# Kernel optimization log

Measured on AMD Instinct MI355X. Metric: run time of the kernel, lower is better.

## Reference

```python
import jax, jax.numpy as jnp
import numpy as np

HID = 4096; NH = 32; NKV = 8; HD = 128; EPS = 1e-6; BASE = 10000.0

def _rmsnorm(x, w):
    # RMSNorm over last (head_dim) axis
    return x * jax.lax.rsqrt(jnp.mean(x * x, axis=-1, keepdims=True) + EPS) * w

def _rope(x, positions):
    # neox-style rotary on (b, s, h, HD): rotate halves
    half = HD // 2
    inv_freq = 1.0 / (BASE ** (jnp.arange(0, HD, 2, dtype=jnp.float32) / HD))  # (half,)
    ang = positions.astype(jnp.float32)[:, None] * inv_freq                    # (s, half)
    cos = jnp.cos(ang)[None, :, None, :]
    sin = jnp.sin(ang)[None, :, None, :]
    x1, x2 = x[..., :half], x[..., half:]
    return jnp.concatenate([x1 * cos - x2 * sin, x2 * cos + x1 * sin], axis=-1)

def setup_inputs() -> dict:
    key = jax.random.key(0)
    k0, k1, k2 = jax.random.split(key, 3)
    b, s = 4, 1024
    return {
        "h_shard": jax.random.normal(k0, (b, s, HID), jnp.float32),
        "positions": jnp.arange(s, dtype=jnp.int32),
        "w_qkv": jax.random.normal(k1, (NH * HD + 2 * NKV * HD, HID), jnp.float32) * 0.02,
        "w_o": jax.random.normal(k2, (HID, NH * HD), jnp.float32) * 0.02,
        "q_norm_w": jnp.ones((HD,), jnp.float32),
        "k_norm_w": jnp.ones((HD,), jnp.float32),
    }

def reference(h_shard, positions, w_qkv, w_o, q_norm_w, k_norm_w):
    b, s, _ = h_shard.shape
    q_sz, kv_sz = NH * HD, NKV * HD
    # fused QKV projection (world_size=1 -> ag_mm is a plain matmul x @ W.T)
    qkv = h_shard @ w_qkv.T                                   # (b, s, q_sz + 2*kv_sz)
    q = qkv[..., :q_sz].reshape(b, s, NH, HD)
    k = qkv[..., q_sz:q_sz + kv_sz].reshape(b, s, NKV, HD)
    v = qkv[..., q_sz + kv_sz:].reshape(b, s, NKV, HD)
    # per-head RMSNorm then RoPE on q/k (Qwen3 ordering)
    q = _rope(_rmsnorm(q, q_norm_w), positions)
    k = _rope(_rmsnorm(k, k_norm_w), positions)
    # GQA SDPA without materializing repeated KV: group query heads per kv head
    g = NH // NKV
    qg = q.reshape(b, s, NKV, g, HD)
    scores = jnp.einsum('bskgd,btkd->bkgst', qg, k) / jnp.sqrt(jnp.float32(HD))
    causal = jnp.tril(jnp.ones((s, s), dtype=bool))
    scores = jnp.where(causal, scores, -jnp.inf)
    probs = jax.nn.softmax(scores, axis=-1)
    attn = jnp.einsum('bkgst,btkd->bskgd', probs, v).reshape(b, s, q_sz)
    # output projection (mm_rs -> plain matmul for world_size=1)
    return attn @ w_o.T
```

## Files before the change

### kernel.cpp

```cpp
#include <hip/hip_runtime.h>

typedef __bf16 bf16;
typedef __bf16 bf16x4 __attribute__((ext_vector_type(4)));
typedef __bf16 bf16x8 __attribute__((ext_vector_type(8)));
typedef float f32x4 __attribute__((ext_vector_type(4)));

#define HID 4096
#define QKV_N 6144
#define NTOK 4096

__device__ __forceinline__ void gload_lds16(const bf16* g, bf16* l) {
  __builtin_amdgcn_global_load_lds(
      (__attribute__((address_space(1))) void*)(g),
      (__attribute__((address_space(3))) void*)(l), 16, 0, 0);
}

__global__ void cvt_kernel(const float4* __restrict__ s, bf16x4* __restrict__ d) {
  int i = blockIdx.x * blockDim.x + threadIdx.x;
  float4 v = s[i];
  bf16x4 o;
  o[0] = (bf16)v.x; o[1] = (bf16)v.y; o[2] = (bf16)v.z; o[3] = (bf16)v.w;
  d[i] = o;
}

template <typename OutT>
__global__ __launch_bounds__(256) void gemm_bt(
    const bf16* __restrict__ A, const bf16* __restrict__ Bm,
    OutT* __restrict__ C, int M, int N, int K)
{
  __shared__ bf16 As[128 * 64];
  __shared__ bf16 Bs[128 * 64];
  const int tid = threadIdx.x;
  const int w = tid >> 6, l = tid & 63;
  const int quad = l >> 4, lane16 = l & 15;
  const int row0 = blockIdx.y * 128, col0 = blockIdx.x * 128;
  const int wm = (w & 1) * 64, wn = (w >> 1) * 64;
  const int lrow = l >> 3;
  const int lkswz = ((l & 7) ^ lrow) * 8;
  const int sw = lane16 & 7;

  f32x4 acc[4][4];
#pragma unroll
  for (int a = 0; a < 4; ++a)
#pragma unroll
    for (int b = 0; b < 4; ++b) acc[a][b] = (f32x4){0.f, 0.f, 0.f, 0.f};

  for (int k0 = 0; k0 < K; k0 += 64) {
#pragma unroll
    for (int r = 0; r < 4; ++r) {
      int i = r * 4 + w;
      gload_lds16(A + (size_t)(row0 + i * 8 + lrow) * K + k0 + lkswz, &As[i * 512 + l * 8]);
      gload_lds16(Bm + (size_t)(col0 + i * 8 + lrow) * K + k0 + lkswz, &Bs[i * 512 + l * 8]);
    }
    __syncthreads();
#pragma unroll
    for (int kk = 0; kk < 2; ++kk) {
      bf16x8 af[4], bfr[4];
#pragma unroll
      for (int im = 0; im < 4; ++im)
        af[im] = *(const bf16x8*)&As[(wm + im * 16 + lane16) * 64 + (((kk * 4 + quad) ^ sw) * 8)];
#pragma unroll
      for (int in_ = 0; in_ < 4; ++in_)
        bfr[in_] = *(const bf16x8*)&Bs[(wn + in_ * 16 + lane16) * 64 + (((kk * 4 + quad) ^ sw) * 8)];
#pragma unroll
      for (int im = 0; im < 4; ++im)
#pragma unroll
        for (int in_ = 0; in_ < 4; ++in_)
          acc[im][in_] = __builtin_amdgcn_mfma_f32_16x16x32_bf16(af[im], bfr[in_], acc[im][in_], 0, 0, 0);
    }
    __syncthreads();
  }
#pragma unroll
  for (int im = 0; im < 4; ++im) {
#pragma unroll
    for (int r = 0; r < 4; ++r) {
      int row = row0 + wm + im * 16 + quad * 4 + r;
      OutT* cp = C + (size_t)row * N + col0 + wn;
#pragma unroll
      for (int in_ = 0; in_ < 4; ++in_)
        cp[in_ * 16 + lane16] = (OutT)acc[im][in_][r];
    }
  }
}

__global__ __launch_bounds__(256) void norm_rope_kernel(
    bf16* __restrict__ qkv, const int* __restrict__ pos,
    const float* __restrict__ qw, const float* __restrict__ kw)
{
  int g = blockIdx.x * 4 + (threadIdx.x >> 6);
  int tok = g / 40;
  int slot = g % 40;
  int d = threadIdx.x & 63;
  bf16* base;
  const float* w;
  if (slot < 32) { base = qkv + (size_t)tok * QKV_N + slot * 128; w = qw; }
  else           { base = qkv + (size_t)tok * QKV_N + HID + (slot - 32) * 128; w = kw; }
  float x1 = (float)base[d], x2 = (float)base[d + 64];
  float ss = x1 * x1 + x2 * x2;
#pragma unroll
  for (int m = 1; m < 64; m <<= 1) ss += __shfl_xor(ss, m, 64);
  float rn = rsqrtf(ss * (1.0f / 128.0f) + 1e-6f);
  x1 = x1 * rn * w[d];
  x2 = x2 * rn * w[d + 64];
  int p = pos[tok & 1023];
  float invf = exp2f(-0.20762050593045952f * (float)d);
  float ang = (float)p * invf;
  float sn, c;
  sincosf(ang, &sn, &c);
  base[d]      = (bf16)(x1 * c - x2 * sn);
  base[d + 64] = (bf16)(x2 * c + x1 * sn);
}

__global__ __launch_bounds__(256) void flash_kernel(
    const bf16* __restrict__ qkv, bf16* __restrict__ attn)
{
  __shared__ bf16 Qs[64 * 128];
  __shared__ bf16 Ks[64 * 128];
  __shared__ bf16 Vt[128 * 72];
  __shared__ bf16 Ps[4][16 * 72];

  const int qt = blockIdx.x;
  const int bh = blockIdx.y;
  const int batch = bh >> 5;
  const int qh = bh & 31;
  const int kvh = qh >> 2;
  const int tid = threadIdx.x;
  const int w = tid >> 6, l = tid & 63;
  const int quad = l >> 4, lane16 = l & 15;
  const int sw = lane16 & 7;
  const size_t tok0 = (size_t)batch * 1024;
  const int q0 = qt * 64;

#pragma unroll
  for (int r = 0; r < 4; ++r) {
    int i = r * 4 + w;
    int rloc = i * 4 + (l >> 4);
    int o = (l & 15) ^ (rloc & 7);
    const bf16* g = qkv + (tok0 + q0 + rloc) * QKV_N + qh * 128 + o * 8;
    gload_lds16(g, &Qs[i * 512 + l * 8]);
  }

  f32x4 O[8];
#pragma unroll
  for (int id = 0; id < 8; ++id) O[id] = (f32x4){0.f, 0.f, 0.f, 0.f};
  float m_run[4], l_run[4];
#pragma unroll
  for (int r = 0; r < 4; ++r) { m_run[r] = -1e30f; l_run[r] = 0.f; }

  const float scale = 0.08838834764831845f;

  for (int j = 0; j <= qt; ++j) {
#pragma unroll
    for (int r = 0; r < 4; ++r) {
      int i = r * 4 + w;
      int rloc = i * 4 + (l >> 4);
      int o = (l & 15) ^ (rloc & 7);
      const bf16* g = qkv + (tok0 + j * 64 + rloc) * QKV_N + HID + kvh * 128 + o * 8;
      gload_lds16(g, &Ks[i * 512 + l * 8]);
    }
#pragma unroll
    for (int c = 0; c < 4; ++c) {
      int dg = c * 4 + w;
      int d0 = dg * 8;
      const bf16* g = qkv + (tok0 + j * 64 + l) * QKV_N + HID + 1024 + kvh * 128 + d0;
      bf16x8 v = *(const bf16x8*)g;
#pragma unroll
      for (int e = 0; e < 8; ++e) Vt[(d0 + e) * 72 + l] = v[e];
    }
    __syncthreads();

    f32x4 s[4];
#pragma unroll
    for (int in_ = 0; in_ < 4; ++in_) s[in_] = (f32x4){0.f, 0.f, 0.f, 0.f};
#pragma unroll
    for (int kk = 0; kk < 4; ++kk) {
      bf16x8 a = *(const bf16x8*)&Qs[(w * 16 + lane16) * 128 + (((kk * 4 + quad) ^ sw) * 8)];
#pragma unroll
      for (int in_ = 0; in_ < 4; ++in_) {
        bf16x8 b = *(const bf16x8*)&Ks[(in_ * 16 + lane16) * 128 + (((kk * 4 + quad) ^ sw) * 8)];
        s[in_] = __builtin_amdgcn_mfma_f32_16x16x32_bf16(a, b, s[in_], 0, 0, 0);
      }
    }

#pragma unroll
    for (int r = 0; r < 4; ++r) {
      int q_abs = q0 + w * 16 + quad * 4 + r;
      float rm = -1e30f;
#pragma unroll
      for (int in_ = 0; in_ < 4; ++in_) {
        int t_abs = j * 64 + in_ * 16 + lane16;
        float v = s[in_][r] * scale;
        v = (t_abs <= q_abs) ? v : -1e30f;
        s[in_][r] = v;
        rm = fmaxf(rm, v);
      }
#pragma unroll
      for (int m = 1; m < 16; m <<= 1) rm = fmaxf(rm, __shfl_xor(rm, m, 64));
      float mn = fmaxf(m_run[r], rm);
      float alpha = __expf(m_run[r] - mn);
      m_run[r] = mn;
      float rs = 0.f;
#pragma unroll
      for (int in_ = 0; in_ < 4; ++in_) {
        float pv = __expf(s[in_][r] - mn);
        s[in_][r] = pv;
        rs += pv;
      }
#pragma unroll
      for (int m = 1; m < 16; m <<= 1) rs += __shfl_xor(rs, m, 64);
      l_run[r] = l_run[r] * alpha + rs;
#pragma unroll
      for (int id = 0; id < 8; ++id) O[id][r] *= alpha;
#pragma unroll
      for (int in_ = 0; in_ < 4; ++in_)
        Ps[w][(quad * 4 + r) * 72 + in_ * 16 + lane16] = (bf16)s[in_][r];
    }

#pragma unroll
    for (int kt = 0; kt < 2; ++kt) {
      bf16x8 a = *(const bf16x8*)&Ps[w][lane16 * 72 + kt * 32 + quad * 8];
#pragma unroll
      for (int id = 0; id < 8; ++id) {
        bf16x8 b = *(const bf16x8*)&Vt[(id * 16 + lane16) * 72 + kt * 32 + quad * 8];
        O[id] = __builtin_amdgcn_mfma_f32_16x16x32_bf16(a, b, O[id], 0, 0, 0);
      }
    }
    __syncthreads();
  }

#pragma unroll
  for (int r = 0; r < 4; ++r) {
    float inv = 1.0f / l_run[r];
    int row = q0 + w * 16 + quad * 4 + r;
    bf16* orow = attn + (tok0 + row) * (size_t)HID + qh * 128;
#pragma unroll
    for (int id = 0; id < 8; ++id) orow[id * 16 + lane16] = (bf16)(O[id][r] * inv);
  }
}

extern "C" void kernel_launch(void* const* d_in, const int* in_sizes, int n_in,
                              void* d_out, int out_size, void* d_ws, size_t ws_size,
                              hipStream_t stream) {
  const float* h    = (const float*)d_in[0];
  const int*   pos  = (const int*)d_in[1];
  const float* wqkv = (const float*)d_in[2];
  const float* wo   = (const float*)d_in[3];
  const float* qw   = (const float*)d_in[4];
  const float* kw   = (const float*)d_in[5];
  float* out = (float*)d_out;

  bf16* hb    = (bf16*)d_ws;
  bf16* wqkvb = hb + 16777216;
  bf16* wob   = wqkvb + 25165824;
  bf16* qkvb  = wob + 16777216;
  bf16* attnb = qkvb + 25165824;

  cvt_kernel<<<16384, 256, 0, stream>>>((const float4*)h, (bf16x4*)hb);
  cvt_kernel<<<24576, 256, 0, stream>>>((const float4*)wqkv, (bf16x4*)wqkvb);
  cvt_kernel<<<16384, 256, 0, stream>>>((const float4*)wo, (bf16x4*)wob);

  gemm_bt<bf16><<<dim3(48, 32), 256, 0, stream>>>(hb, wqkvb, qkvb, NTOK, QKV_N, HID);

  norm_rope_kernel<<<NTOK * 40 / 4, 256, 0, stream>>>(qkvb, pos, qw, kw);

  flash_kernel<<<dim3(16, 128), 256, 0, stream>>>(qkvb, attnb);

  gemm_bt<float><<<dim3(32, 32), 256, 0, stream>>>(attnb, wob, out, NTOK, HID, HID);
}
```

Measured before the change: 875.0 us.

## Double-buffer K/V in flash attention and keep Q fragments in registers

The flash attention kernel now double-buffers K and V tiles in LDS, prefetching the next K via async global-to-LDS loads and the next V into registers while the current tile computes. Q fragments are held in registers instead of LDS, V transpose uses an XOR-swizzled layout without padding, causal masking runs only on the diagonal tile, and the q-tile order is reversed for half the heads to balance causal work. This aims to hide global load latency and cut LDS traffic and barriers, at the cost of more LDS and registers, which may lower occupancy.

```diff
diff --git a/kernel.cpp b/kernel.cpp
--- a/kernel.cpp
+++ b/kernel.cpp
@@ -114,13 +114,12 @@
 __global__ __launch_bounds__(256) void flash_kernel(
     const bf16* __restrict__ qkv, bf16* __restrict__ attn)
 {
-  __shared__ bf16 Qs[64 * 128];
-  __shared__ bf16 Ks[64 * 128];
-  __shared__ bf16 Vt[128 * 72];
+  __shared__ bf16 Ks[2][64 * 128];
+  __shared__ bf16 Vt[2][128 * 64];
   __shared__ bf16 Ps[4][16 * 72];
 
-  const int qt = blockIdx.x;
   const int bh = blockIdx.y;
+  const int qt = ((bh >> 4) & 1) ? (15 - blockIdx.x) : blockIdx.x;
   const int batch = bh >> 5;
   const int qh = bh & 31;
   const int kvh = qh >> 2;
@@ -131,13 +130,11 @@
   const size_t tok0 = (size_t)batch * 1024;
   const int q0 = qt * 64;
 
-#pragma unroll
-  for (int r = 0; r < 4; ++r) {
-    int i = r * 4 + w;
-    int rloc = i * 4 + (l >> 4);
-    int o = (l & 15) ^ (rloc & 7);
-    const bf16* g = qkv + (tok0 + q0 + rloc) * QKV_N + qh * 128 + o * 8;
-    gload_lds16(g, &Qs[i * 512 + l * 8]);
+  bf16x8 qf[4];
+  {
+    const bf16* qrow = qkv + (tok0 + q0 + w * 16 + lane16) * QKV_N + qh * 128 + quad * 8;
+#pragma unroll
+    for (int kk = 0; kk < 4; ++kk) qf[kk] = *(const bf16x8*)(qrow + kk * 32);
   }
 
   f32x4 O[8];
@@ -148,49 +145,72 @@
   for (int r = 0; r < 4; ++r) { m_run[r] = -1e30f; l_run[r] = 0.f; }
 
   const float scale = 0.08838834764831845f;
-
-  for (int j = 0; j <= qt; ++j) {
+  bf16x8 vreg[4];
+
+  auto stage_K = [&](int j, int buf) {
 #pragma unroll
     for (int r = 0; r < 4; ++r) {
       int i = r * 4 + w;
       int rloc = i * 4 + (l >> 4);
       int o = (l & 15) ^ (rloc & 7);
       const bf16* g = qkv + (tok0 + j * 64 + rloc) * QKV_N + HID + kvh * 128 + o * 8;
-      gload_lds16(g, &Ks[i * 512 + l * 8]);
-    }
+      gload_lds16(g, &Ks[buf][i * 512 + l * 8]);
+    }
+  };
+  auto load_V = [&](int j) {
 #pragma unroll
     for (int c = 0; c < 4; ++c) {
-      int dg = c * 4 + w;
-      int d0 = dg * 8;
-      const bf16* g = qkv + (tok0 + j * 64 + l) * QKV_N + HID + 1024 + kvh * 128 + d0;
-      bf16x8 v = *(const bf16x8*)g;
-#pragma unroll
-      for (int e = 0; e < 8; ++e) Vt[(d0 + e) * 72 + l] = v[e];
-    }
-    __syncthreads();
+      int d0 = (c * 4 + w) * 8;
+      vreg[c] = *(const bf16x8*)(qkv + (tok0 + j * 64 + l) * QKV_N + HID + 1024 + kvh * 128 + d0);
+    }
+  };
+  auto write_V = [&](int buf) {
+#pragma unroll
+    for (int c = 0; c < 4; ++c) {
+      int d0 = (c * 4 + w) * 8;
+#pragma unroll
+      for (int e = 0; e < 8; ++e) {
+        int d = d0 + e;
+        Vt[buf][d * 64 + (((l >> 3) ^ (d & 7)) * 8) + (l & 7)] = vreg[c][e];
+      }
+    }
+  };
+
+  stage_K(0, 0);
+  load_V(0);
+  write_V(0);
+  __syncthreads();
+
+  for (int j = 0; j <= qt; ++j) {
+    const int p = j & 1;
+    if (j < qt) { stage_K(j + 1, p ^ 1); load_V(j + 1); }
 
     f32x4 s[4];
 #pragma unroll
     for (int in_ = 0; in_ < 4; ++in_) s[in_] = (f32x4){0.f, 0.f, 0.f, 0.f};
 #pragma unroll
     for (int kk = 0; kk < 4; ++kk) {
-      bf16x8 a = *(const bf16x8*)&Qs[(w * 16 + lane16) * 128 + (((kk * 4 + quad) ^ sw) * 8)];
 #pragma unroll
       for (int in_ = 0; in_ < 4; ++in_) {
-        bf16x8 b = *(const bf16x8*)&Ks[(in_ * 16 + lane16) * 128 + (((kk * 4 + quad) ^ sw) * 8)];
-        s[in_] = __builtin_amdgcn_mfma_f32_16x16x32_bf16(a, b, s[in_], 0, 0, 0);
-      }
-    }
-
-#pragma unroll
-    for (int r = 0; r < 4; ++r) {
-      int q_abs = q0 + w * 16 + quad * 4 + r;
+        bf16x8 b = *(const bf16x8*)&Ks[p][(in_ * 16 + lane16) * 128 + (((kk * 4 + quad) ^ sw) * 8)];
+        s[in_] = __builtin_amdgcn_mfma_f32_16x16x32_bf16(qf[kk], b, s[in_], 0, 0, 0);
+      }
+    }
+
+    if (j < qt) write_V(p ^ 1);
+
+    const bool edge = (j == qt);
+#pragma unroll
+    for (int r = 0; r < 4; ++r) {
       float rm = -1e30f;
 #pragma unroll
       for (int in_ = 0; in_ < 4; ++in_) {
-        int t_abs = j * 64 + in_ * 16 + lane16;
         float v = s[in_][r] * scale;
-        v = (t_abs <= q_abs) ? v : -1e30f;
+        if (edge) {
+          int t_abs = j * 64 + in_ * 16 + lane16;
+          int q_abs = q0 + w * 16 + quad * 4 + r;
+          v = (t_abs <= q_abs) ? v : -1e30f;
+        }
         s[in_][r] = v;
         rm = fmaxf(rm, v);
       }
@@ -221,7 +241,7 @@
       bf16x8 a = *(const bf16x8*)&Ps[w][lane16 * 72 + kt * 32 + quad * 8];
 #pragma unroll
       for (int id = 0; id < 8; ++id) {
-        bf16x8 b = *(const bf16x8*)&Vt[(id * 16 + lane16) * 72 + kt * 32 + quad * 8];
+        bf16x8 b = *(const bf16x8*)&Vt[p][(id * 16 + lane16) * 64 + (((kt * 4 + quad) ^ sw) * 8)];
         O[id] = __builtin_amdgcn_mfma_f32_16x16x32_bf16(a, b, O[id], 0, 0, 0);
       }
     }
```

After: 808.4 us. 7.6% less time.
